# Kernel tuning notes

Measured on AMD Instinct MI355X. Metric: run time of the kernel, lower is better.

Reference implementation:

```python
import jax, jax.numpy as jnp
import numpy as np

THRESHOLD = 0.1
NMS_KERNEL = 7
TOP_K = 200
THING_LIST = (11, 12, 13, 14, 15, 16, 17, 18)


def setup_inputs() -> dict:
    key = jax.random.key(0)
    k1, k2, k3 = jax.random.split(key, 3)
    H, W = 512, 1024
    semantic_pred = jax.random.randint(k1, (1, H, W), 0, 19, dtype=jnp.int32)
    ctr_hmp = jax.random.uniform(k2, (1, 1, H, W), dtype=jnp.float32)
    offsets = jax.random.normal(k3, (1, 2, H, W), dtype=jnp.float32)
    return {"semantic_pred": semantic_pred, "ctr_hmp": ctr_hmp, "offsets": offsets}


def _find_instance_center(ctr_hmp):
    # ctr_hmp: [1,1,H,W]. Threshold -> -1, max-pool NMS, fixed-size top-k.
    hmp = jnp.where(ctr_hmp > THRESHOLD, ctr_hmp, jnp.float32(-1.0))
    pad = (NMS_KERNEL - 1) // 2
    pooled = jax.lax.reduce_window(
        hmp, -jnp.inf, jax.lax.max,
        (1, 1, NMS_KERNEL, NMS_KERNEL), (1, 1, 1, 1),
        [(0, 0), (0, 0), (pad, pad), (pad, pad)])
    hmp = jnp.where(hmp == pooled, hmp, jnp.float32(-1.0))[0, 0]  # [H,W]
    H, W = hmp.shape
    flat = hmp.reshape(-1)
    scores, idx = jax.lax.top_k(flat, TOP_K)          # fixed K centers (jit-safe)
    valid = scores > 0                                 # torch keeps only score > 0
    # restore row-major (torch.nonzero) ordering among valid centers
    order_key = jnp.where(valid, idx, flat.shape[0])
    sort_ord = jnp.argsort(order_key)
    idx = idx[sort_ord]
    valid = valid[sort_ord]
    ctr = jnp.stack([idx // W, idx % W], axis=-1)      # [K,2] (y, x)
    return ctr, valid


def reference(semantic_pred, ctr_hmp, offsets):
    H, W = offsets.shape[2], offsets.shape[3]
    ctr, valid = _find_instance_center(ctr_hmp)
    dt = offsets.dtype
    # pixel -> predicted center location (coord + offset), flattened to [HW]
    y = jnp.arange(H, dtype=dt)
    x = jnp.arange(W, dtype=dt)
    loc_y = (y[:, None] + offsets[0, 0]).reshape(-1)
    loc_x = (x[None, :] + offsets[0, 1]).reshape(-1)
    cy = jnp.where(valid, ctr[:, 0].astype(dt), jnp.asarray(1e10, dt))
    cx = jnp.where(valid, ctr[:, 1].astype(dt), jnp.asarray(1e10, dt))
    # squared distance has the same argmin as torch.norm; avoid (K,HW,2) tensor
    d2 = (cy[:, None] - loc_y[None, :]) ** 2 + (cx[:, None] - loc_x[None, :]) ** 2  # [K,HW]
    instance_id = jnp.argmin(d2, axis=0).astype(semantic_pred.dtype).reshape(1, H, W) + 1
    thing_seg = jnp.isin(semantic_pred, jnp.asarray(THING_LIST, dtype=semantic_pred.dtype))
    instance = jnp.where(thing_seg, instance_id, 0)
    # centers padded to fixed K; invalid rows flagged by `valid`
    center = ctr[None]  # [1,K,2]
    return instance, center, valid
```

## Files before the change

### kernel.cpp

```cpp
#include <hip/hip_runtime.h>
#include <math.h>

#define HH 512
#define WW 1024
#define HW (HH*WW)
#define TOPK 200
#define NMSPAD 3
#define THRESH 0.1f
#define NBINS 4096
#define SUBCAP 1024
#define SLOTS 24
#define NBX 32
#define NBY 64
#define NB (NBX*NBY)

__device__ __forceinline__ int score_bin(float s) {
    int b = (int)((s - THRESH) * (float)(NBINS / 0.9f));
    if (b < 0) b = 0;
    if (b > NBINS - 1) b = NBINS - 1;
    return b;
}

__global__ __launch_bounds__(256) void k1_nms(const float* __restrict__ hmp,
                                              int* __restrict__ blkcnt,
                                              float* __restrict__ blkscore,
                                              int* __restrict__ blkidx) {
    const int BX = 32, BY = 8, TW = BX + 6, TH = BY + 6;
    __shared__ float A[TH][TW + 2];
    __shared__ float R[TH][BX];
    __shared__ float lsc[SLOTS];
    __shared__ int   lid[SLOTS];
    __shared__ int   s_cnt;
    int lx = threadIdx.x, ly = threadIdx.y;
    int x0 = blockIdx.x * BX, y0 = blockIdx.y * BY;
    int tid = ly * BX + lx;
    if (tid == 0) s_cnt = 0;

    for (int t = tid; t < TH * TW; t += 256) {
        int r = t / TW, c = t % TW;
        int gy = y0 - NMSPAD + r, gx = x0 - NMSPAD + c;
        float v = -INFINITY;
        if (gy >= 0 && gy < HH && gx >= 0 && gx < WW) {
            float h = hmp[gy * WW + gx];
            v = (h > THRESH) ? h : -1.0f;
        }
        A[r][c] = v;
    }
    __syncthreads();
    for (int t = tid; t < TH * BX; t += 256) {
        int r = t / BX, c = t % BX;
        float m = A[r][c];
        #pragma unroll
        for (int d = 1; d < 7; ++d) m = fmaxf(m, A[r][c + d]);
        R[r][c] = m;
    }
    __syncthreads();
    float v = A[ly + NMSPAD][lx + NMSPAD];
    if (v > 0.0f) {
        float m = R[ly][lx];
        #pragma unroll
        for (int d = 1; d < 7; ++d) m = fmaxf(m, R[ly + d][lx]);
        if (v == m) {
            int p = atomicAdd(&s_cnt, 1);
            if (p < SLOTS) { lsc[p] = v; lid[p] = (y0 + ly) * WW + (x0 + lx); }
        }
    }
    __syncthreads();
    int b = blockIdx.y * NBX + blockIdx.x;
    int cnt = min(s_cnt, SLOTS);
    if (tid == 0) blkcnt[b] = cnt;
    if (tid < cnt) {
        blkscore[b * SLOTS + tid] = lsc[tid];
        blkidx[b * SLOTS + tid] = lid[tid];
    }
}

__global__ __launch_bounds__(1024) void k3_select(const int* __restrict__ blkcnt,
                                                  const float* __restrict__ blkscore,
                                                  const int* __restrict__ blkidx,
                                                  int* __restrict__ out_center,
                                                  int* __restrict__ out_valid,
                                                  float2* __restrict__ ctr2) {
    __shared__ int hist[NBINS];
    __shared__ int chunk[1024];
    __shared__ float ss[SUBCAP];
    __shared__ int sidx[SUBCAP];
    __shared__ int srank[SUBCAP];
    __shared__ int sselidx[TOPK];
    __shared__ int s_cb, s_m, s_V;
    int tid = threadIdx.x;

    #pragma unroll
    for (int i = 0; i < NBINS / 1024; ++i) hist[tid + i * 1024] = 0;
    if (tid == 0) { s_m = 0; s_V = 0; }
    __syncthreads();

    int myv = 0;
    for (int b = tid; b < NB; b += 1024) {
        int cnt = blkcnt[b];
        myv += cnt;
        for (int s = 0; s < cnt; ++s)
            atomicAdd(&hist[score_bin(blkscore[b * SLOTS + s])], 1);
    }
    if (myv) atomicAdd(&s_V, myv);
    __syncthreads();

    int base = tid * (NBINS / 1024), sum = 0;
    #pragma unroll
    for (int i = 0; i < NBINS / 1024; ++i) sum += hist[base + i];
    chunk[tid] = sum;
    __syncthreads();

    if (tid == 0) {
        int acc = 0, cb = 0;
        for (int c = 1023; c >= 0; --c) {
            if (acc + chunk[c] >= TOPK) {
                for (int b = c * (NBINS / 1024) + (NBINS / 1024) - 1;
                     b >= c * (NBINS / 1024); --b) {
                    acc += hist[b];
                    if (acc >= TOPK) { cb = b; break; }
                }
                break;
            }
            acc += chunk[c];
        }
        s_cb = cb;
    }
    __syncthreads();
    int cb = s_cb;
    int V = s_V;

    for (int b = tid; b < NB; b += 1024) {
        int cnt = blkcnt[b];
        for (int s = 0; s < cnt; ++s) {
            float sc = blkscore[b * SLOTS + s];
            if (score_bin(sc) >= cb) {
                int p = atomicAdd(&s_m, 1);
                if (p < SUBCAP) { ss[p] = sc; sidx[p] = blkidx[b * SLOTS + s]; }
            }
        }
    }
    __syncthreads();
    int m = min(s_m, SUBCAP);

    for (int i = tid; i < m; i += 1024) {
        float si = ss[i]; int ii = sidx[i]; int r = 0;
        for (int j = 0; j < m; ++j) {
            float sj = ss[j];
            r += (sj > si) || (sj == si && sidx[j] < ii);
        }
        srank[i] = r;
    }
    __syncthreads();

    for (int i = tid; i < m; i += 1024) {
        if (srank[i] < TOPK) {
            int ii = sidx[i];
            int pos = 0;
            for (int j = 0; j < m; ++j)
                pos += (srank[j] < TOPK) && (sidx[j] < ii);
            int y = ii >> 10, x = ii & (WW - 1);
            out_center[2 * pos] = y;
            out_center[2 * pos + 1] = x;
            out_valid[pos] = 1;
            ctr2[pos] = make_float2((float)y, (float)x);
            sselidx[pos] = ii;
        }
    }
    __syncthreads();

    if (tid == 0 && V < TOPK) {
        int slot = V, t = 0, p = 0;
        while (slot < TOPK) {
            if (p < V && t == sselidx[p]) { t++; p++; }
            else {
                out_center[2 * slot] = t >> 10;
                out_center[2 * slot + 1] = t & (WW - 1);
                out_valid[slot] = 0;
                ctr2[slot] = make_float2(1e10f, 1e10f);
                t++; slot++;
            }
        }
    }
}

__global__ __launch_bounds__(256) void k4_assign(const int* __restrict__ sem,
                                                 const float* __restrict__ off,
                                                 const float2* __restrict__ ctr2,
                                                 int* __restrict__ out_inst) {
    __shared__ float2 c[TOPK];
    int tid = threadIdx.x;
    if (tid < TOPK) c[tid] = ctr2[tid];
    __syncthreads();

    int p = blockIdx.x * 256 + tid;
    int y = p >> 10, x = p & (WW - 1);
    int s = sem[p];
    float ly = __fadd_rn((float)y, off[p]);
    float lx = __fadd_rn((float)x, off[HW + p]);

    float ymin = ly, ymax = ly, xmin = lx, xmax = lx;
    #pragma unroll
    for (int mdist = 32; mdist >= 1; mdist >>= 1) {
        ymin = fminf(ymin, __shfl_xor(ymin, mdist, 64));
        ymax = fmaxf(ymax, __shfl_xor(ymax, mdist, 64));
        xmin = fminf(xmin, __shfl_xor(xmin, mdist, 64));
        xmax = fmaxf(xmax, __shfl_xor(xmax, mdist, 64));
    }

    int lane = tid & 63;
    float ub = INFINITY;
    float lbv[4];
    #pragma unroll
    for (int r = 0; r < 4; ++r) {
        int k = r * 64 + lane;
        float lb = INFINITY;
        float u = INFINITY;
        if (k < TOPK) {
            float2 ck = c[k];
            float dyM = fmaxf(__fsub_rn(ck.x, ymin), __fsub_rn(ymax, ck.x));
            float dxM = fmaxf(__fsub_rn(ck.y, xmin), __fsub_rn(xmax, ck.y));
            u = __fadd_rn(__fmul_rn(dyM, dyM), __fmul_rn(dxM, dxM));
            float dyL = fmaxf(0.0f, fmaxf(__fsub_rn(ck.x, ymax), __fsub_rn(ymin, ck.x)));
            float dxL = fmaxf(0.0f, fmaxf(__fsub_rn(ck.y, xmax), __fsub_rn(xmin, ck.y)));
            lb = __fadd_rn(__fmul_rn(dyL, dyL), __fmul_rn(dxL, dxL));
        }
        ub = fminf(ub, u);
        lbv[r] = lb;
    }
    #pragma unroll
    for (int mdist = 32; mdist >= 1; mdist >>= 1)
        ub = fminf(ub, __shfl_xor(ub, mdist, 64));

    unsigned long long km[4];
    #pragma unroll
    for (int r = 0; r < 4; ++r) km[r] = __ballot(lbv[r] <= ub);
    if (!(km[0] | km[1] | km[2] | km[3])) {
        km[0] = km[1] = km[2] = ~0ull; km[3] = 0xFFull;
    }

    float best = INFINITY;
    int bid = 0;
    #pragma unroll
    for (int r = 0; r < 4; ++r) {
        unsigned long long msk = km[r];
        while (msk) {
            int k = r * 64 + __builtin_ctzll(msk);
            msk &= msk - 1;
            float2 ck = c[k];
            float dy = __fsub_rn(ck.x, ly);
            float dx = __fsub_rn(ck.y, lx);
            float d2 = __fadd_rn(__fmul_rn(dy, dy), __fmul_rn(dx, dx));
            if (d2 < best) { best = d2; bid = k; }
        }
    }
    unsigned t = (unsigned)(s - 11);
    out_inst[p] = (t <= 7u) ? (bid + 1) : 0;
}

extern "C" void kernel_launch(void* const* d_in, const int* in_sizes, int n_in,
                              void* d_out, int out_size, void* d_ws, size_t ws_size,
                              hipStream_t stream) {
    const int* sem = (const int*)d_in[0];
    const float* hmp = (const float*)d_in[1];
    const float* off = (const float*)d_in[2];
    int* out = (int*)d_out;

    char* ws = (char*)d_ws;
    int* blkcnt     = (int*)(ws);
    float* blkscore = (float*)(ws + 8192);
    int* blkidx     = (int*)(ws + 204800);
    float2* ctr2    = (float2*)(ws + 401408);

    int* out_inst = out;
    int* out_center = out + HW;
    int* out_valid = out + HW + 2 * TOPK;

    k1_nms<<<dim3(NBX, NBY), dim3(32, 8), 0, stream>>>(hmp, blkcnt, blkscore,
                                                       blkidx);
    k3_select<<<1, 1024, 0, stream>>>(blkcnt, blkscore, blkidx,
                                      out_center, out_valid, ctr2);
    k4_assign<<<HW / 256, 256, 0, stream>>>(sem, off, ctr2, out_inst);
}
```

Measured before the change: 102.2 us.

## Cache NMS candidates in LDS and parallelize top-k threshold scan

Packs score and index into a single int2 record per candidate and has the single-block select kernel compute block offsets with a wave-level prefix scan. It then caches all candidates in shared memory so the second filtering pass reads LDS instead of global memory. The serial single-thread cutoff search over the histogram becomes a parallel prefix scan. A fallback re-reads global memory if the candidate count exceeds the cache capacity, and the larger shared-memory footprint is the main added cost.

```diff
diff --git a/kernel.cpp b/kernel.cpp
--- a/kernel.cpp
+++ b/kernel.cpp
@@ -9,6 +9,7 @@
 #define THRESH 0.1f
 #define NBINS 4096
 #define SUBCAP 1024
+#define CACHECAP 12288
 #define SLOTS 24
 #define NBX 32
 #define NBY 64
@@ -23,8 +24,7 @@
 
 __global__ __launch_bounds__(256) void k1_nms(const float* __restrict__ hmp,
                                               int* __restrict__ blkcnt,
-                                              float* __restrict__ blkscore,
-                                              int* __restrict__ blkidx) {
+                                              int2* __restrict__ blkpair) {
     const int BX = 32, BY = 8, TW = BX + 6, TH = BY + 6;
     __shared__ float A[TH][TW + 2];
     __shared__ float R[TH][BX];
@@ -69,74 +69,128 @@
     int b = blockIdx.y * NBX + blockIdx.x;
     int cnt = min(s_cnt, SLOTS);
     if (tid == 0) blkcnt[b] = cnt;
-    if (tid < cnt) {
-        blkscore[b * SLOTS + tid] = lsc[tid];
-        blkidx[b * SLOTS + tid] = lid[tid];
-    }
+    if (tid < cnt)
+        blkpair[b * SLOTS + tid] = make_int2(__float_as_int(lsc[tid]), lid[tid]);
 }
 
 __global__ __launch_bounds__(1024) void k3_select(const int* __restrict__ blkcnt,
-                                                  const float* __restrict__ blkscore,
-                                                  const int* __restrict__ blkidx,
+                                                  const int2* __restrict__ blkpair,
                                                   int* __restrict__ out_center,
                                                   int* __restrict__ out_valid,
                                                   float2* __restrict__ ctr2) {
-    __shared__ int hist[NBINS];
-    __shared__ int chunk[1024];
+    __shared__ int   hist[NBINS];
+    __shared__ float cs[CACHECAP];
+    __shared__ int   ci[CACHECAP];
     __shared__ float ss[SUBCAP];
-    __shared__ int sidx[SUBCAP];
-    __shared__ int srank[SUBCAP];
-    __shared__ int sselidx[TOPK];
-    __shared__ int s_cb, s_m, s_V;
+    __shared__ int   sidx[SUBCAP];
+    __shared__ int   srank[SUBCAP];
+    __shared__ int   sselidx[TOPK];
+    __shared__ int   sb[64];
+    __shared__ int   s_cb, s_m, s_ovf, s_T0, s_V;
     int tid = threadIdx.x;
+    int lane = tid & 63, wid = tid >> 6;
 
     #pragma unroll
     for (int i = 0; i < NBINS / 1024; ++i) hist[tid + i * 1024] = 0;
-    if (tid == 0) { s_m = 0; s_V = 0; }
-    __syncthreads();
-
-    int myv = 0;
-    for (int b = tid; b < NB; b += 1024) {
-        int cnt = blkcnt[b];
-        myv += cnt;
-        for (int s = 0; s < cnt; ++s)
-            atomicAdd(&hist[score_bin(blkscore[b * SLOTS + s])], 1);
-    }
-    if (myv) atomicAdd(&s_V, myv);
-    __syncthreads();
-
-    int base = tid * (NBINS / 1024), sum = 0;
-    #pragma unroll
-    for (int i = 0; i < NBINS / 1024; ++i) sum += hist[base + i];
-    chunk[tid] = sum;
-    __syncthreads();
-
-    if (tid == 0) {
-        int acc = 0, cb = 0;
-        for (int c = 1023; c >= 0; --c) {
-            if (acc + chunk[c] >= TOPK) {
-                for (int b = c * (NBINS / 1024) + (NBINS / 1024) - 1;
-                     b >= c * (NBINS / 1024); --b) {
-                    acc += hist[b];
-                    if (acc >= TOPK) { cb = b; break; }
-                }
-                break;
-            }
-            acc += chunk[c];
-        }
-        s_cb = cb;
+    if (tid == 0) { s_m = 0; s_ovf = 0; s_cb = 0; }
+
+    int c0 = blkcnt[tid];
+    int c1 = blkcnt[tid + 1024];
+    int v0 = c0, v1 = c1;
+    #pragma unroll
+    for (int off = 1; off < 64; off <<= 1) {
+        int u0 = __shfl_up(v0, off, 64);
+        int u1 = __shfl_up(v1, off, 64);
+        if (lane >= off) { v0 += u0; v1 += u1; }
+    }
+    if (lane == 63) { sb[wid] = v0; sb[16 + wid] = v1; }
+    __syncthreads();
+    if (tid < 16) {
+        int w0 = sb[tid], w1 = sb[16 + tid];
+        int a0 = w0, a1 = w1;
+        #pragma unroll
+        for (int off = 1; off < 16; off <<= 1) {
+            int u0 = __shfl_up(a0, off, 64);
+            int u1 = __shfl_up(a1, off, 64);
+            if (lane >= off) { a0 += u0; a1 += u1; }
+        }
+        sb[32 + tid] = a0 - w0;
+        sb[48 + tid] = a1 - w1;
+        if (tid == 15) { s_T0 = a0; s_V = a0 + a1; }
+    }
+    __syncthreads();
+    int off0 = sb[32 + wid] + v0 - c0;
+    int off1 = s_T0 + sb[48 + wid] + v1 - c1;
+    int V = s_V;
+
+    for (int rep = 0; rep < 2; ++rep) {
+        int b   = rep ? tid + 1024 : tid;
+        int cnt = rep ? c1 : c0;
+        int off = rep ? off1 : off0;
+        for (int s = 0; s < cnt; ++s) {
+            int2 pr = blkpair[b * SLOTS + s];
+            float sc = __int_as_float(pr.x);
+            atomicAdd(&hist[score_bin(sc)], 1);
+            int p = off + s;
+            if (p < CACHECAP) { cs[p] = sc; ci[p] = pr.y; }
+            else s_ovf = 1;
+        }
+    }
+    __syncthreads();
+
+    int base = tid * (NBINS / 1024);
+    int csum = 0;
+    #pragma unroll
+    for (int i = 0; i < NBINS / 1024; ++i) csum += hist[base + i];
+    int vc = csum;
+    #pragma unroll
+    for (int off = 1; off < 64; off <<= 1) {
+        int u = __shfl_up(vc, off, 64);
+        if (lane >= off) vc += u;
+    }
+    if (lane == 63) sb[wid] = vc;
+    __syncthreads();
+    if (tid < 16) {
+        int w = sb[tid]; int a = w;
+        #pragma unroll
+        for (int off = 1; off < 16; off <<= 1) {
+            int u = __shfl_up(a, off, 64);
+            if (lane >= off) a += u;
+        }
+        sb[32 + tid] = a - w;
+    }
+    __syncthreads();
+    int pexcl = sb[32 + wid] + vc - csum;
+    int S = V - pexcl;
+    if (S >= TOPK && S - csum < TOPK) {
+        int acc = S - csum;
+        for (int bb = base + NBINS / 1024 - 1; bb >= base; --bb) {
+            acc += hist[bb];
+            if (acc >= TOPK) { s_cb = bb; break; }
+        }
     }
     __syncthreads();
     int cb = s_cb;
-    int V = s_V;
-
-    for (int b = tid; b < NB; b += 1024) {
-        int cnt = blkcnt[b];
-        for (int s = 0; s < cnt; ++s) {
-            float sc = blkscore[b * SLOTS + s];
+
+    if (!s_ovf) {
+        for (int i = tid; i < V; i += 1024) {
+            float sc = cs[i];
             if (score_bin(sc) >= cb) {
                 int p = atomicAdd(&s_m, 1);
-                if (p < SUBCAP) { ss[p] = sc; sidx[p] = blkidx[b * SLOTS + s]; }
+                if (p < SUBCAP) { ss[p] = sc; sidx[p] = ci[i]; }
+            }
+        }
+    } else {
+        for (int rep = 0; rep < 2; ++rep) {
+            int b   = rep ? tid + 1024 : tid;
+            int cnt = rep ? c1 : c0;
+            for (int s = 0; s < cnt; ++s) {
+                int2 pr = blkpair[b * SLOTS + s];
+                float sc = __int_as_float(pr.x);
+                if (score_bin(sc) >= cb) {
+                    int p = atomicAdd(&s_m, 1);
+                    if (p < SUBCAP) { ss[p] = sc; sidx[p] = pr.y; }
+                }
             }
         }
     }
@@ -267,18 +321,16 @@
     int* out = (int*)d_out;
 
     char* ws = (char*)d_ws;
-    int* blkcnt     = (int*)(ws);
-    float* blkscore = (float*)(ws + 8192);
-    int* blkidx     = (int*)(ws + 204800);
-    float2* ctr2    = (float2*)(ws + 401408);
+    int* blkcnt   = (int*)(ws);
+    int2* blkpair = (int2*)(ws + 8192);
+    float2* ctr2  = (float2*)(ws + 8192 + 393216);
 
     int* out_inst = out;
     int* out_center = out + HW;
     int* out_valid = out + HW + 2 * TOPK;
 
-    k1_nms<<<dim3(NBX, NBY), dim3(32, 8), 0, stream>>>(hmp, blkcnt, blkscore,
-                                                       blkidx);
-    k3_select<<<1, 1024, 0, stream>>>(blkcnt, blkscore, blkidx,
+    k1_nms<<<dim3(NBX, NBY), dim3(32, 8), 0, stream>>>(hmp, blkcnt, blkpair);
+    k3_select<<<1, 1024, 0, stream>>>(blkcnt, blkpair,
                                       out_center, out_valid, ctr2);
     k4_assign<<<HW / 256, 256, 0, stream>>>(sem, off, ctr2, out_inst);
 }
```

New measurement: 93.41 us. 1.09x faster.
